# Performance work log

Hardware: AMD Instinct MI355X
Metric: run time of the kernel (lower is better)

The kernel has to match this reference:

```python
import jax, jax.numpy as jnp
import numpy as np

X_SCALE, X_ZP = 0.03, -66      # int8 quant params (qmin=-128, qmax=127)
Y_SCALE, Y_ZP = 0.025, 160     # uint8 quant params (qmin=0, qmax=255)
M = K = N = 4096


def setup_inputs() -> dict:
    key = jax.random.key(0)
    kx, ky = jax.random.split(key)
    # x holds int8-range values [-128, 127], y holds uint8-range values [0, 255]
    x = jax.random.randint(kx, (M, K), -128, 128, dtype=jnp.int32)
    y = jax.random.randint(ky, (K, N), 0, 256, dtype=jnp.int32)
    return {"x": x, "y": y}


def reference(x, y):
    # dequantize_per_tensor: (q - zero_point) * scale  (values already in [qmin, qmax])
    xf = (x.astype(jnp.float32) - X_ZP) * X_SCALE   # [M, K]
    yf = (y.astype(jnp.float32) - Y_ZP) * Y_SCALE   # [K, N]
    return jnp.matmul(xf, yf)                       # [M, N]
```

## Files before the change

kernel.cpp:

```cpp
#include <hip/hip_runtime.h>
#include <stdint.h>

#define Mdim 4096
#define Kdim 4096
#define Ndim 4096

typedef __attribute__((ext_vector_type(4))) int v4i;
typedef __attribute__((ext_vector_type(16))) int v16i;

__device__ __forceinline__ void gload_lds16(const void* g, void* l) {
  __builtin_amdgcn_global_load_lds(
      (__attribute__((address_space(1))) void*)(uintptr_t)g,
      (__attribute__((address_space(3))) void*)(uint32_t)(uintptr_t)l,
      16, 0, 0);
}

__global__ __launch_bounds__(256) void pack_x_kernel(const int* __restrict__ x,
                                                     char* __restrict__ x8,
                                                     int* __restrict__ rsx) {
  const int row = blockIdx.x;
  const int t = threadIdx.x;
  const int4* src = (const int4*)(x + (size_t)row * Kdim) + t * 4;
  int sum = 0;
  int p[4];
#pragma unroll
  for (int i = 0; i < 4; ++i) {
    int4 v = src[i];
    sum += v.x + v.y + v.z + v.w;
    p[i] = (v.x & 0xff) | ((v.y & 0xff) << 8) | ((v.z & 0xff) << 16) | (v.w << 24);
  }
  ((int4*)x8)[(size_t)row * 256 + t] = make_int4(p[0], p[1], p[2], p[3]);
#pragma unroll
  for (int o = 32; o > 0; o >>= 1) sum += __shfl_down(sum, o, 64);
  __shared__ int red[4];
  if ((t & 63) == 0) red[t >> 6] = sum;
  __syncthreads();
  if (t == 0) rsx[row] = red[0] + red[1] + red[2] + red[3];
}

__global__ __launch_bounds__(256) void pack_yt_kernel(const int* __restrict__ y,
                                                      char* __restrict__ yt,
                                                      int* __restrict__ csy) {
  __shared__ int wtile[64 * 24];
  __shared__ int psum[4][64];
  const int t = threadIdx.x;
  const int n0 = blockIdx.x * 64;
  const int k0 = blockIdx.y * 64;
  const int nl = t & 63;
  const int rq = t >> 6;
  int s = 0;
#pragma unroll
  for (int it = 0; it < 4; ++it) {
    const int q = rq + it * 4;
    int v0 = y[(size_t)(k0 + q * 4 + 0) * Ndim + n0 + nl];
    int v1 = y[(size_t)(k0 + q * 4 + 1) * Ndim + n0 + nl];
    int v2 = y[(size_t)(k0 + q * 4 + 2) * Ndim + n0 + nl];
    int v3 = y[(size_t)(k0 + q * 4 + 3) * Ndim + n0 + nl];
    v0 -= 128; v1 -= 128; v2 -= 128; v3 -= 128;
    s += v0 + v1 + v2 + v3;
    wtile[nl * 24 + q] = (v0 & 0xff) | ((v1 & 0xff) << 8) | ((v2 & 0xff) << 16) | (v3 << 24);
  }
  psum[rq][nl] = s;
  __syncthreads();
  const int orow = t >> 2;
  const int cw = t & 3;
  int4 wv = *(const int4*)(wtile + orow * 24 + cw * 4);
  *(int4*)(yt + (size_t)(n0 + orow) * Kdim + k0 + cw * 16) = wv;
  if (t < 64) {
    int tot = psum[0][t] + psum[1][t] + psum[2][t] + psum[3][t];
    atomicAdd(csy + n0 + t, tot);
  }
}

__global__ __launch_bounds__(256, 1) void gemm_i8_kernel(
    const char* __restrict__ A, const char* __restrict__ B,
    const int* __restrict__ rsx, const int* __restrict__ csy,
    float* __restrict__ out) {
  __shared__ __align__(16) char lds[2 * 32768];
  const int t = threadIdx.x;
  const int l = t & 63;
  const int w = t >> 6;
  const int wr = w >> 1;
  const int wc = w & 1;
  const int bm = blockIdx.y * 256;
  const int bn = blockIdx.x * 256;

  v16i acc[4][4];
#pragma unroll
  for (int i = 0; i < 4; ++i)
#pragma unroll
    for (int j = 0; j < 4; ++j)
#pragma unroll
      for (int q = 0; q < 16; ++q) acc[i][j][q] = 0;

  const int srow = t >> 2;
  const int cswz = ((t & 3) ^ ((t >> 3) & 3)) * 16;
  const char* gA = A + (size_t)(bm + srow) * Kdim + cswz;
  const char* gB = B + (size_t)(bn + srow) * Kdim + cswz;

#define STAGE(buf_off, koff)                                                  \
  do {                                                                        \
    _Pragma("unroll") for (int i = 0; i < 4; ++i)                             \
        gload_lds16(gA + (koff) + (size_t)i * 64 * Kdim,                      \
                    lds + (buf_off) + i * 4096 + t * 16);                     \
    _Pragma("unroll") for (int i = 0; i < 4; ++i)                             \
        gload_lds16(gB + (koff) + (size_t)i * 64 * Kdim,                      \
                    lds + (buf_off) + 16384 + i * 4096 + t * 16);             \
  } while (0)

  const int arow = wr * 128 + (l & 31);
  const int brow = wc * 128 + (l & 31);
  const int lhalf = l >> 5;
  const int lkey = (l >> 1) & 3;

#define COMPUTE(buf_off)                                                      \
  do {                                                                        \
    const char* As = lds + (buf_off);                                         \
    const char* Bs = lds + (buf_off) + 16384;                                 \
    _Pragma("unroll") for (int ks = 0; ks < 2; ++ks) {                        \
      const int slot = ((ks * 2 + lhalf) ^ lkey) * 16;                        \
      v4i a[4], b[4];                                                         \
      _Pragma("unroll") for (int i = 0; i < 4; ++i)                           \
          a[i] = *(const v4i*)(As + (arow + i * 32) * 64 + slot);             \
      _Pragma("unroll") for (int j = 0; j < 4; ++j)                           \
          b[j] = *(const v4i*)(Bs + (brow + j * 32) * 64 + slot);             \
      _Pragma("unroll") for (int i = 0; i < 4; ++i)                           \
          _Pragma("unroll") for (int j = 0; j < 4; ++j)                       \
              acc[i][j] = __builtin_amdgcn_mfma_i32_32x32x32_i8(              \
                  a[i], b[j], acc[i][j], 0, 0, 0);                            \
    }                                                                         \
  } while (0)

  STAGE(0, 0);
  __syncthreads();
  for (int kt = 0; kt < 64; kt += 2) {
    if (kt + 1 < 64) STAGE(32768, (kt + 1) * 64);
    COMPUTE(0);
    __syncthreads();
    if (kt + 2 < 64) STAGE(0, (kt + 2) * 64);
    COMPUTE(32768);
    __syncthreads();
  }

  const int col = l & 31;
#pragma unroll
  for (int i = 0; i < 4; ++i) {
    const int gm0 = bm + wr * 128 + i * 32;
#pragma unroll
    for (int j = 0; j < 4; ++j) {
      const int gn = bn + wc * 128 + j * 32 + col;
      const int cs = 66 * csy[gn] - 8650752;
#pragma unroll
      for (int r = 0; r < 16; ++r) {
        const int row = (r & 3) + 8 * (r >> 2) + 4 * lhalf;
        const int gm = gm0 + row;
        const int val = acc[i][j][r] - 32 * rsx[gm] + cs;
        out[(size_t)gm * Ndim + gn] = 7.5e-4f * (float)val;
      }
    }
  }
#undef STAGE
#undef COMPUTE
}

extern "C" void kernel_launch(void* const* d_in, const int* in_sizes, int n_in,
                              void* d_out, int out_size, void* d_ws, size_t ws_size,
                              hipStream_t stream) {
  (void)in_sizes; (void)n_in; (void)out_size; (void)ws_size;
  const int* x = (const int*)d_in[0];
  const int* y = (const int*)d_in[1];
  float* out = (float*)d_out;
  char* ws = (char*)d_ws;
  char* x8 = ws;
  char* yt = ws + (size_t)Mdim * Kdim;
  int* rsx = (int*)(ws + (size_t)Mdim * Kdim + (size_t)Kdim * Ndim);
  int* csy = rsx + Mdim;

  hipMemsetAsync(csy, 0, Ndim * sizeof(int), stream);
  pack_x_kernel<<<Mdim, 256, 0, stream>>>(x, x8, rsx);
  pack_yt_kernel<<<dim3(Ndim / 64, Kdim / 64), 256, 0, stream>>>(y, yt, csy);
  gemm_i8_kernel<<<dim3(Ndim / 256, Mdim / 256), 256, 0, stream>>>(x8, yt, rsx, csy, out);
}
```

Measured before the change: 256.9 us.

## Use 8-wave GEMM blocks, coalesce x packing, vectorize y transpose-pack

The GEMM block grows from 4 to 8 waves. Each wave now covers a 64x128 sub-tile with half the accumulators, and launch bounds allow two blocks per CU, so more waves are available to hide LDS and global latency. pack_x now uses fully coalesced strided int4 loads and dword stores. pack_yt loads int4 rows, packs bytes into a padded LDS tile, and does the byte transpose in registers, computing column sums with shuffles. The cost is fewer MFMAs per A/B fragment load per wave, which raises LDS traffic relative to compute.

```diff
diff --git a/kernel.cpp b/kernel.cpp
--- a/kernel.cpp
+++ b/kernel.cpp
@@ -20,16 +20,16 @@
                                                      int* __restrict__ rsx) {
   const int row = blockIdx.x;
   const int t = threadIdx.x;
-  const int4* src = (const int4*)(x + (size_t)row * Kdim) + t * 4;
+  const int4* src = (const int4*)(x + (size_t)row * Kdim);
+  int* dst = (int*)(x8 + (size_t)row * Kdim);
   int sum = 0;
-  int p[4];
 #pragma unroll
   for (int i = 0; i < 4; ++i) {
-    int4 v = src[i];
+    int4 v = src[t + 256 * i];
     sum += v.x + v.y + v.z + v.w;
-    p[i] = (v.x & 0xff) | ((v.y & 0xff) << 8) | ((v.z & 0xff) << 16) | (v.w << 24);
+    dst[t + 256 * i] =
+        (v.x & 0xff) | ((v.y & 0xff) << 8) | ((v.z & 0xff) << 16) | (v.w << 24);
   }
-  ((int4*)x8)[(size_t)row * 256 + t] = make_int4(p[0], p[1], p[2], p[3]);
 #pragma unroll
   for (int o = 32; o > 0; o >>= 1) sum += __shfl_down(sum, o, 64);
   __shared__ int red[4];
@@ -41,38 +41,46 @@
 __global__ __launch_bounds__(256) void pack_yt_kernel(const int* __restrict__ y,
                                                       char* __restrict__ yt,
                                                       int* __restrict__ csy) {
-  __shared__ int wtile[64 * 24];
-  __shared__ int psum[4][64];
+  __shared__ int wt[64 * 17];
   const int t = threadIdx.x;
   const int n0 = blockIdx.x * 64;
   const int k0 = blockIdx.y * 64;
-  const int nl = t & 63;
-  const int rq = t >> 6;
-  int s = 0;
+  const int c = t & 15;
+  const int r0 = t >> 4;
 #pragma unroll
-  for (int it = 0; it < 4; ++it) {
-    const int q = rq + it * 4;
-    int v0 = y[(size_t)(k0 + q * 4 + 0) * Ndim + n0 + nl];
-    int v1 = y[(size_t)(k0 + q * 4 + 1) * Ndim + n0 + nl];
-    int v2 = y[(size_t)(k0 + q * 4 + 2) * Ndim + n0 + nl];
-    int v3 = y[(size_t)(k0 + q * 4 + 3) * Ndim + n0 + nl];
-    v0 -= 128; v1 -= 128; v2 -= 128; v3 -= 128;
-    s += v0 + v1 + v2 + v3;
-    wtile[nl * 24 + q] = (v0 & 0xff) | ((v1 & 0xff) << 8) | ((v2 & 0xff) << 16) | (v3 << 24);
+  for (int s = 0; s < 4; ++s) {
+    const int r = r0 + s * 16;
+    int4 v = *(const int4*)(y + (size_t)(k0 + r) * Ndim + n0 + c * 4);
+    v.x -= 128; v.y -= 128; v.z -= 128; v.w -= 128;
+    wt[r * 17 + c] =
+        (v.x & 0xff) | ((v.y & 0xff) << 8) | ((v.z & 0xff) << 16) | (v.w << 24);
   }
-  psum[rq][nl] = s;
   __syncthreads();
-  const int orow = t >> 2;
-  const int cw = t & 3;
-  int4 wv = *(const int4*)(wtile + orow * 24 + cw * 4);
-  *(int4*)(yt + (size_t)(n0 + orow) * Kdim + k0 + cw * 16) = wv;
-  if (t < 64) {
-    int tot = psum[0][t] + psum[1][t] + psum[2][t] + psum[3][t];
-    atomicAdd(csy + n0 + t, tot);
+  const int n = t >> 2;
+  const int kq = t & 3;
+  const int colw = n >> 2;
+  const int byi = (n & 3) * 8;
+  int outw[4];
+  int bsum = 0;
+#pragma unroll
+  for (int j = 0; j < 4; ++j) {
+    int b[4];
+#pragma unroll
+    for (int jj = 0; jj < 4; ++jj) {
+      const int word = wt[(kq * 16 + j * 4 + jj) * 17 + colw];
+      b[jj] = (word >> byi) & 0xff;
+      bsum += (int)(char)b[jj];
+    }
+    outw[j] = b[0] | (b[1] << 8) | (b[2] << 16) | (b[3] << 24);
   }
+  *(int4*)(yt + (size_t)(n0 + n) * Kdim + k0 + kq * 16) =
+      make_int4(outw[0], outw[1], outw[2], outw[3]);
+  bsum += __shfl_xor(bsum, 1, 64);
+  bsum += __shfl_xor(bsum, 2, 64);
+  if (kq == 0) atomicAdd(csy + n0 + n, bsum);
 }
 
-__global__ __launch_bounds__(256, 1) void gemm_i8_kernel(
+__global__ __launch_bounds__(512, 2) void gemm_i8_kernel(
     const char* __restrict__ A, const char* __restrict__ B,
     const int* __restrict__ rsx, const int* __restrict__ csy,
     float* __restrict__ out) {
@@ -80,14 +88,14 @@
   const int t = threadIdx.x;
   const int l = t & 63;
   const int w = t >> 6;
-  const int wr = w >> 1;
-  const int wc = w & 1;
+  const int warow = w >> 1;
+  const int wbcol = w & 1;
   const int bm = blockIdx.y * 256;
   const int bn = blockIdx.x * 256;
 
-  v16i acc[4][4];
+  v16i acc[2][4];
 #pragma unroll
-  for (int i = 0; i < 4; ++i)
+  for (int i = 0; i < 2; ++i)
 #pragma unroll
     for (int j = 0; j < 4; ++j)
 #pragma unroll
@@ -100,16 +108,16 @@
 
 #define STAGE(buf_off, koff)                                                  \
   do {                                                                        \
-    _Pragma("unroll") for (int i = 0; i < 4; ++i)                             \
-        gload_lds16(gA + (koff) + (size_t)i * 64 * Kdim,                      \
-                    lds + (buf_off) + i * 4096 + t * 16);                     \
-    _Pragma("unroll") for (int i = 0; i < 4; ++i)                             \
-        gload_lds16(gB + (koff) + (size_t)i * 64 * Kdim,                      \
-                    lds + (buf_off) + 16384 + i * 4096 + t * 16);             \
+    _Pragma("unroll") for (int i = 0; i < 2; ++i)                             \
+        gload_lds16(gA + (koff) + (size_t)i * 128 * Kdim,                     \
+                    lds + (buf_off) + i * 8192 + t * 16);                     \
+    _Pragma("unroll") for (int i = 0; i < 2; ++i)                             \
+        gload_lds16(gB + (koff) + (size_t)i * 128 * Kdim,                     \
+                    lds + (buf_off) + 16384 + i * 8192 + t * 16);             \
   } while (0)
 
-  const int arow = wr * 128 + (l & 31);
-  const int brow = wc * 128 + (l & 31);
+  const int arow = warow * 64 + (l & 31);
+  const int brow = wbcol * 128 + (l & 31);
   const int lhalf = l >> 5;
   const int lkey = (l >> 1) & 3;
 
@@ -119,12 +127,12 @@
     const char* Bs = lds + (buf_off) + 16384;                                 \
     _Pragma("unroll") for (int ks = 0; ks < 2; ++ks) {                        \
       const int slot = ((ks * 2 + lhalf) ^ lkey) * 16;                        \
-      v4i a[4], b[4];                                                         \
-      _Pragma("unroll") for (int i = 0; i < 4; ++i)                           \
+      v4i a[2], b[4];                                                         \
+      _Pragma("unroll") for (int i = 0; i < 2; ++i)                           \
           a[i] = *(const v4i*)(As + (arow + i * 32) * 64 + slot);             \
       _Pragma("unroll") for (int j = 0; j < 4; ++j)                           \
           b[j] = *(const v4i*)(Bs + (brow + j * 32) * 64 + slot);             \
-      _Pragma("unroll") for (int i = 0; i < 4; ++i)                           \
+      _Pragma("unroll") for (int i = 0; i < 2; ++i)                           \
           _Pragma("unroll") for (int j = 0; j < 4; ++j)                       \
               acc[i][j] = __builtin_amdgcn_mfma_i32_32x32x32_i8(              \
                   a[i], b[j], acc[i][j], 0, 0, 0);                            \
@@ -144,11 +152,11 @@
 
   const int col = l & 31;
 #pragma unroll
-  for (int i = 0; i < 4; ++i) {
-    const int gm0 = bm + wr * 128 + i * 32;
+  for (int i = 0; i < 2; ++i) {
+    const int gm0 = bm + warow * 64 + i * 32;
 #pragma unroll
     for (int j = 0; j < 4; ++j) {
-      const int gn = bn + wc * 128 + j * 32 + col;
+      const int gn = bn + wbcol * 128 + j * 32 + col;
       const int cs = 66 * csy[gn] - 8650752;
 #pragma unroll
       for (int r = 0; r < 16; ++r) {
@@ -179,5 +187,5 @@
   hipMemsetAsync(csy, 0, Ndim * sizeof(int), stream);
   pack_x_kernel<<<Mdim, 256, 0, stream>>>(x, x8, rsx);
   pack_yt_kernel<<<dim3(Ndim / 64, Kdim / 64), 256, 0, stream>>>(y, yt, csy);
-  gemm_i8_kernel<<<dim3(Ndim / 256, Mdim / 256), 256, 0, stream>>>(x8, yt, rsx, csy, out);
+  gemm_i8_kernel<<<dim3(Ndim / 256, Mdim / 256), 512, 0, stream>>>(x8, yt, rsx, csy, out);
 }
```

Result: faster. 244.0 us (-5.0%).
